# Optimization experiments

Hardware: AMD Instinct MI355X
Metric: run time of the kernel (lower is better)

## Reference

```python
import jax, jax.numpy as jnp
import numpy as np

N_NODES = 50000
N_EDGES = 800000
D_IN = 64
D_OUT = 64


def setup_inputs() -> dict:
    key = jax.random.key(0)
    ks = jax.random.split(key, 7)
    feat = jax.random.normal(ks[0], (N_NODES, D_IN), dtype=jnp.float32)
    src = jax.random.randint(ks[1], (N_EDGES,), 0, N_NODES, dtype=jnp.int32)
    dst = jax.random.randint(ks[2], (N_EDGES,), 0, N_NODES, dtype=jnp.int32)
    W_self = jax.random.normal(ks[3], (D_OUT, D_IN), dtype=jnp.float32) * 0.1
    b_self = jax.random.normal(ks[4], (D_OUT,), dtype=jnp.float32) * 0.1
    W_neigh = jax.random.normal(ks[5], (D_OUT, D_IN), dtype=jnp.float32) * 0.1
    b_neigh = jax.random.normal(ks[6], (D_OUT,), dtype=jnp.float32) * 0.1
    return {"feat": feat, "src": src, "dst": dst, "W_self": W_self,
            "b_self": b_self, "W_neigh": W_neigh, "b_neigh": b_neigh,
            "act_flag": 1}


def reference(feat, src, dst, W_self, b_self, W_neigh, b_neigh, act_flag):
    n = feat.shape[0]
    # update_all(copy_src('h','m'), mean('m','neigh')):
    # gather src features along edges, segment-sum into dst, divide by in-degree
    msgs = feat[src]  # [E, D_in]
    neigh_sum = jax.ops.segment_sum(msgs, dst, num_segments=n)  # [N, D_in]
    deg = jax.ops.segment_sum(jnp.ones((dst.shape[0],), feat.dtype), dst,
                              num_segments=n)  # [N]
    h_neigh = jnp.where(deg[:, None] > 0, neigh_sum / jnp.maximum(deg, 1.0)[:, None], 0.0)
    # include=True: h_self = feat (dst nodes == all nodes)
    rst = feat @ W_self.T + b_self + h_neigh @ W_neigh.T + b_neigh
    if act_flag:
        rst = jax.nn.relu(rst)
    return rst
```

## Files before the change

kernel.cpp:

```cpp
#include <hip/hip_runtime.h>


#define N_NODES 50000
#define N_EDGES 800000
#define D 64
#define NPB 64
#define SCAN_BLOCK 1024
#define NUM_SCAN_BLOCKS ((N_NODES + SCAN_BLOCK - 1) / SCAN_BLOCK)

__global__ __launch_bounds__(256) void k_hist(const int* __restrict__ dst,
                                              int* __restrict__ deg,
                                              int* __restrict__ rank)
{
    const int e4 = blockIdx.x * 256 + threadIdx.x;
    if (e4 >= N_EDGES / 4) return;
    const int4 d = *reinterpret_cast<const int4*>(dst + e4 * 4);
    int4 r;
    r.x = atomicAdd(&deg[d.x], 1);
    r.y = atomicAdd(&deg[d.y], 1);
    r.z = atomicAdd(&deg[d.z], 1);
    r.w = atomicAdd(&deg[d.w], 1);
    *reinterpret_cast<int4*>(rank + e4 * 4) = r;
}

__global__ __launch_bounds__(SCAN_BLOCK) void k_scan_blocks(
    const int* __restrict__ deg,
    int* __restrict__ row_start,
    int* __restrict__ blocksums)
{
    __shared__ int s[SCAN_BLOCK];
    const int t = threadIdx.x;
    const int i = blockIdx.x * SCAN_BLOCK + t;
    const int orig = (i < N_NODES) ? deg[i] : 0;
    s[t] = orig;
    __syncthreads();
    for (int off = 1; off < SCAN_BLOCK; off <<= 1) {
        const int add = (t >= off) ? s[t - off] : 0;
        __syncthreads();
        s[t] += add;
        __syncthreads();
    }
    if (i < N_NODES) row_start[i] = s[t] - orig;
    if (t == SCAN_BLOCK - 1) blocksums[blockIdx.x] = s[t];
}

__global__ __launch_bounds__(SCAN_BLOCK) void k_scan_add(
    int* __restrict__ row_start, const int* __restrict__ blocksums)
{
    __shared__ int bs[64];
    const int t = threadIdx.x;
    if (t < 64) bs[t] = (t < NUM_SCAN_BLOCKS) ? blocksums[t] : 0;
    __syncthreads();
    int offset = 0;
    for (int k = 0; k < (int)blockIdx.x; ++k) offset += bs[k];
    const int i = blockIdx.x * SCAN_BLOCK + t;
    if (i < N_NODES) row_start[i] += offset;
}

__global__ __launch_bounds__(256) void k_fill(const int* __restrict__ src,
                                              const int* __restrict__ dst,
                                              const int* __restrict__ rank,
                                              const int* __restrict__ row_start,
                                              int* __restrict__ src_sorted)
{
    const int e4 = blockIdx.x * 256 + threadIdx.x;
    if (e4 >= N_EDGES / 4) return;
    const int4 s = *reinterpret_cast<const int4*>(src + e4 * 4);
    const int4 d = *reinterpret_cast<const int4*>(dst + e4 * 4);
    const int4 r = *reinterpret_cast<const int4*>(rank + e4 * 4);
    src_sorted[row_start[d.x] + r.x] = s.x;
    src_sorted[row_start[d.y] + r.y] = s.y;
    src_sorted[row_start[d.z] + r.z] = s.z;
    src_sorted[row_start[d.w] + r.w] = s.w;
}

__global__ __launch_bounds__(256) void k_fused(
    const float* __restrict__ feat,
    const int* __restrict__ row_start,
    const int* __restrict__ deg,
    const int* __restrict__ src_sorted,
    const float* __restrict__ W_self,
    const float* __restrict__ b_self,
    const float* __restrict__ W_neigh,
    const float* __restrict__ b_neigh,
    const int* __restrict__ act_flag,
    float* __restrict__ out)
{
    __shared__ float fT[D][NPB + 1];
    __shared__ float hT[D][NPB + 1];

    const int tid  = threadIdx.x;
    const int lane = tid & 63;
    const int w    = __builtin_amdgcn_readfirstlane(tid >> 6);
    const int n_base = blockIdx.x * NPB;

    #pragma unroll
    for (int r = 0; r < 16; ++r) {
        const int idx = r * 256 + tid;
        const int nl  = idx >> 6;
        const int i   = idx & 63;
        const int n   = n_base + nl;
        fT[i][nl] = (n < N_NODES) ? feat[n * D + i] : 0.0f;
    }

    const int slot = lane >> 4;
    const int d4   = (lane & 15) << 2;
    for (int q = 0; q < 16; ++q) {
        const int nl = (w << 4) + q;
        const int n  = n_base + nl;
        float4 a = make_float4(0.f, 0.f, 0.f, 0.f);
        int dg = 0;
        if (n < N_NODES) {
            const int start = row_start[n];
            dg = deg[n];
            int my_idx = 0;
            if (lane < dg) my_idx = src_sorted[start + lane];
            const int kmax  = (dg < 64) ? dg : 64;
            const int iters = (kmax + 3) >> 2;
            #pragma unroll 2
            for (int t2 = 0; t2 < iters; ++t2) {
                const int k  = (t2 << 2) + slot;
                const int kc = (k < kmax) ? k : 0;
                const int s  = __shfl(my_idx, kc);
                const float m = (k < kmax) ? 1.0f : 0.0f;
                const float4 v = *reinterpret_cast<const float4*>(feat + s * D + d4);
                a.x = fmaf(m, v.x, a.x);
                a.y = fmaf(m, v.y, a.y);
                a.z = fmaf(m, v.z, a.z);
                a.w = fmaf(m, v.w, a.w);
            }
            for (int k = 64 + slot; k < dg; k += 4) {
                const int s = src_sorted[start + k];
                const float4 v = *reinterpret_cast<const float4*>(feat + s * D + d4);
                a.x += v.x; a.y += v.y; a.z += v.z; a.w += v.w;
            }
        }
        a.x += __shfl_xor(a.x, 16); a.x += __shfl_xor(a.x, 32);
        a.y += __shfl_xor(a.y, 16); a.y += __shfl_xor(a.y, 32);
        a.z += __shfl_xor(a.z, 16); a.z += __shfl_xor(a.z, 32);
        a.w += __shfl_xor(a.w, 16); a.w += __shfl_xor(a.w, 32);
        const float inv = (dg > 0) ? (1.0f / (float)dg) : 0.0f;
        const float v = (slot & 1) ? ((slot & 2) ? a.w : a.y)
                                   : ((slot & 2) ? a.z : a.x);
        hT[d4 + slot][nl] = v * inv;
    }
    __syncthreads();

    const int nl = lane;
    const int act = act_flag[0];
    float acc[16];
    #pragma unroll
    for (int jj = 0; jj < 16; ++jj) {
        const int j = (w << 4) + jj;
        acc[jj] = b_self[j] + b_neigh[j];
    }
    #pragma unroll
    for (int c = 0; c < 4; ++c) {
        float fr[16], hr[16];
        #pragma unroll
        for (int u = 0; u < 16; ++u) {
            fr[u] = fT[c * 16 + u][nl];
            hr[u] = hT[c * 16 + u][nl];
        }
        #pragma unroll
        for (int jj = 0; jj < 16; ++jj) {
            const int j = (w << 4) + jj;
            const float* ws = &W_self [j * D + c * 16];
            const float* wn = &W_neigh[j * D + c * 16];
            #pragma unroll
            for (int u = 0; u < 16; ++u) {
                acc[jj] = fmaf(fr[u], ws[u], acc[jj]);
                acc[jj] = fmaf(hr[u], wn[u], acc[jj]);
            }
        }
    }

    __syncthreads();
    #pragma unroll
    for (int jj = 0; jj < 16; ++jj) {
        float o = acc[jj];
        o = act ? fmaxf(o, 0.0f) : o;
        fT[(w << 4) + jj][nl] = o;
    }
    __syncthreads();
    #pragma unroll
    for (int r = 0; r < 16; ++r) {
        const int idx = r * 256 + tid;
        const int nl2 = idx >> 6;
        const int j   = idx & 63;
        const int n2  = n_base + nl2;
        if (n2 < N_NODES) out[n2 * D + j] = fT[j][nl2];
    }
}

extern "C" void kernel_launch(void* const* d_in, const int* in_sizes, int n_in,
                              void* d_out, int out_size, void* d_ws, size_t ws_size,
                              hipStream_t stream)
{
    const float* feat    = (const float*)d_in[0];
    const int*   src     = (const int*)  d_in[1];
    const int*   dst     = (const int*)  d_in[2];
    const float* W_self  = (const float*)d_in[3];
    const float* b_self  = (const float*)d_in[4];
    const float* W_neigh = (const float*)d_in[5];
    const float* b_neigh = (const float*)d_in[6];
    const int*   actf    = (const int*)  d_in[7];
    float* out = (float*)d_out;

    char* base = (char*)d_ws;
    int* deg        = (int*)(base);
    int* row_start  = (int*)(base + 200000);
    int* blocksums  = (int*)(base + 400000);
    int* rank       = (int*)(base + 400256);
    int* src_sorted = (int*)(base + 3600256);

    hipMemsetAsync(deg, 0, 200000, stream);

    const int e4blocks = (N_EDGES / 4 + 255) / 256;
    k_hist<<<e4blocks, 256, 0, stream>>>(dst, deg, rank);
    k_scan_blocks<<<NUM_SCAN_BLOCKS, SCAN_BLOCK, 0, stream>>>(deg, row_start, blocksums);
    k_scan_add<<<NUM_SCAN_BLOCKS, SCAN_BLOCK, 0, stream>>>(row_start, blocksums);
    k_fill<<<e4blocks, 256, 0, stream>>>(src, dst, rank, row_start, src_sorted);

    const int fblocks = (N_NODES + NPB - 1) / NPB;
    k_fused<<<fblocks, 256, 0, stream>>>(feat, row_start, deg, src_sorted,
                                         W_self, b_self, W_neigh, b_neigh,
                                         actf, out);
}
```

Measured before the change: 195.6 us.

## Replace scan-add pass with tiny block-prefix scan; double fused kernel threads

```diff
diff --git a/kernel.cpp b/kernel.cpp
--- a/kernel.cpp
+++ b/kernel.cpp
@@ -5,6 +5,7 @@
 #define N_EDGES 800000
 #define D 64
 #define NPB 64
+#define TPB 512
 #define SCAN_BLOCK 1024
 #define NUM_SCAN_BLOCKS ((N_NODES + SCAN_BLOCK - 1) / SCAN_BLOCK)
 
@@ -44,23 +45,25 @@
     if (t == SCAN_BLOCK - 1) blocksums[blockIdx.x] = s[t];
 }
 
-__global__ __launch_bounds__(SCAN_BLOCK) void k_scan_add(
-    int* __restrict__ row_start, const int* __restrict__ blocksums)
-{
-    __shared__ int bs[64];
+__global__ __launch_bounds__(64) void k_scan_l2(const int* __restrict__ blocksums,
+                                                int* __restrict__ bs_prefix)
+{
     const int t = threadIdx.x;
-    if (t < 64) bs[t] = (t < NUM_SCAN_BLOCKS) ? blocksums[t] : 0;
-    __syncthreads();
-    int offset = 0;
-    for (int k = 0; k < (int)blockIdx.x; ++k) offset += bs[k];
-    const int i = blockIdx.x * SCAN_BLOCK + t;
-    if (i < N_NODES) row_start[i] += offset;
+    const int orig = (t < NUM_SCAN_BLOCKS) ? blocksums[t] : 0;
+    int v = orig;
+    #pragma unroll
+    for (int off = 1; off < 64; off <<= 1) {
+        const int u = __shfl_up(v, off);
+        if (t >= off) v += u;
+    }
+    if (t < NUM_SCAN_BLOCKS) bs_prefix[t] = v - orig;
 }
 
 __global__ __launch_bounds__(256) void k_fill(const int* __restrict__ src,
                                               const int* __restrict__ dst,
                                               const int* __restrict__ rank,
                                               const int* __restrict__ row_start,
+                                              const int* __restrict__ bs_prefix,
                                               int* __restrict__ src_sorted)
 {
     const int e4 = blockIdx.x * 256 + threadIdx.x;
@@ -68,15 +71,16 @@
     const int4 s = *reinterpret_cast<const int4*>(src + e4 * 4);
     const int4 d = *reinterpret_cast<const int4*>(dst + e4 * 4);
     const int4 r = *reinterpret_cast<const int4*>(rank + e4 * 4);
-    src_sorted[row_start[d.x] + r.x] = s.x;
-    src_sorted[row_start[d.y] + r.y] = s.y;
-    src_sorted[row_start[d.z] + r.z] = s.z;
-    src_sorted[row_start[d.w] + r.w] = s.w;
-}
-
-__global__ __launch_bounds__(256) void k_fused(
+    src_sorted[row_start[d.x] + bs_prefix[d.x >> 10] + r.x] = s.x;
+    src_sorted[row_start[d.y] + bs_prefix[d.y >> 10] + r.y] = s.y;
+    src_sorted[row_start[d.z] + bs_prefix[d.z >> 10] + r.z] = s.z;
+    src_sorted[row_start[d.w] + bs_prefix[d.w >> 10] + r.w] = s.w;
+}
+
+__global__ __launch_bounds__(TPB) void k_fused(
     const float* __restrict__ feat,
     const int* __restrict__ row_start,
+    const int* __restrict__ bs_prefix,
     const int* __restrict__ deg,
     const int* __restrict__ src_sorted,
     const float* __restrict__ W_self,
@@ -95,8 +99,8 @@
     const int n_base = blockIdx.x * NPB;
 
     #pragma unroll
-    for (int r = 0; r < 16; ++r) {
-        const int idx = r * 256 + tid;
+    for (int r = 0; r < 8; ++r) {
+        const int idx = r * TPB + tid;
         const int nl  = idx >> 6;
         const int i   = idx & 63;
         const int n   = n_base + nl;
@@ -105,13 +109,13 @@
 
     const int slot = lane >> 4;
     const int d4   = (lane & 15) << 2;
-    for (int q = 0; q < 16; ++q) {
-        const int nl = (w << 4) + q;
+    for (int q = 0; q < 8; ++q) {
+        const int nl = (w << 3) + q;
         const int n  = n_base + nl;
         float4 a = make_float4(0.f, 0.f, 0.f, 0.f);
         int dg = 0;
         if (n < N_NODES) {
-            const int start = row_start[n];
+            const int start = row_start[n] + bs_prefix[n >> 10];
             dg = deg[n];
             int my_idx = 0;
             if (lane < dg) my_idx = src_sorted[start + lane];
@@ -148,10 +152,10 @@
 
     const int nl = lane;
     const int act = act_flag[0];
-    float acc[16];
-    #pragma unroll
-    for (int jj = 0; jj < 16; ++jj) {
-        const int j = (w << 4) + jj;
+    float acc[8];
+    #pragma unroll
+    for (int jj = 0; jj < 8; ++jj) {
+        const int j = (w << 3) + jj;
         acc[jj] = b_self[j] + b_neigh[j];
     }
     #pragma unroll
@@ -163,8 +167,8 @@
             hr[u] = hT[c * 16 + u][nl];
         }
         #pragma unroll
-        for (int jj = 0; jj < 16; ++jj) {
-            const int j = (w << 4) + jj;
+        for (int jj = 0; jj < 8; ++jj) {
+            const int j = (w << 3) + jj;
             const float* ws = &W_self [j * D + c * 16];
             const float* wn = &W_neigh[j * D + c * 16];
             #pragma unroll
@@ -177,15 +181,15 @@
 
     __syncthreads();
     #pragma unroll
-    for (int jj = 0; jj < 16; ++jj) {
+    for (int jj = 0; jj < 8; ++jj) {
         float o = acc[jj];
         o = act ? fmaxf(o, 0.0f) : o;
-        fT[(w << 4) + jj][nl] = o;
-    }
-    __syncthreads();
-    #pragma unroll
-    for (int r = 0; r < 16; ++r) {
-        const int idx = r * 256 + tid;
+        fT[(w << 3) + jj][nl] = o;
+    }
+    __syncthreads();
+    #pragma unroll
+    for (int r = 0; r < 8; ++r) {
+        const int idx = r * TPB + tid;
         const int nl2 = idx >> 6;
         const int j   = idx & 63;
         const int n2  = n_base + nl2;
@@ -211,19 +215,20 @@
     int* deg        = (int*)(base);
     int* row_start  = (int*)(base + 200000);
     int* blocksums  = (int*)(base + 400000);
-    int* rank       = (int*)(base + 400256);
-    int* src_sorted = (int*)(base + 3600256);
+    int* bs_prefix  = (int*)(base + 400256);
+    int* rank       = (int*)(base + 400512);
+    int* src_sorted = (int*)(base + 3600512);
 
     hipMemsetAsync(deg, 0, 200000, stream);
 
     const int e4blocks = (N_EDGES / 4 + 255) / 256;
     k_hist<<<e4blocks, 256, 0, stream>>>(dst, deg, rank);
     k_scan_blocks<<<NUM_SCAN_BLOCKS, SCAN_BLOCK, 0, stream>>>(deg, row_start, blocksums);
-    k_scan_add<<<NUM_SCAN_BLOCKS, SCAN_BLOCK, 0, stream>>>(row_start, blocksums);
-    k_fill<<<e4blocks, 256, 0, stream>>>(src, dst, rank, row_start, src_sorted);
+    k_scan_l2<<<1, 64, 0, stream>>>(blocksums, bs_prefix);
+    k_fill<<<e4blocks, 256, 0, stream>>>(src, dst, rank, row_start, bs_prefix, src_sorted);
 
     const int fblocks = (N_NODES + NPB - 1) / NPB;
-    k_fused<<<fblocks, 256, 0, stream>>>(feat, row_start, deg, src_sorted,
+    k_fused<<<fblocks, TPB, 0, stream>>>(feat, row_start, bs_prefix, deg, src_sorted,
                                          W_self, b_self, W_neigh, b_neigh,
                                          actf, out);
 }
```

Result: no change. 195.6 us (-0.0%).
